# Performance work log

Hardware: AMD Instinct MI355X
Metric: run time of the kernel (lower is better)

The kernel has to match this reference:

```python
import jax, jax.numpy as jnp
import numpy as np

NEG_BIG = 10000000000.0  # matches tf source's -1e10 mask fill


def setup_inputs() -> dict:
    key = jax.random.key(0)
    k1, k2, k3 = jax.random.split(key, 3)
    B, H, T, D = 2, 12, 4096, 64
    return {
        "q": jax.random.normal(k1, (B, H, T, D), dtype=jnp.float32),
        "k": jax.random.normal(k2, (B, H, T, D), dtype=jnp.float32),
        "v": jax.random.normal(k3, (B, H, T, D), dtype=jnp.float32),
        "localAttention": 256,
    }


def _band_mask(nd, ns, local_attention, dtype):
    # 1's in the lower triangle counting from the lower-right corner,
    # optionally restricted to a local window of width `local_attention`.
    i = jnp.arange(nd)[:, None]
    j = jnp.arange(ns)[None, :]
    m = i >= j - ns + nd
    if local_attention > 0:
        m = m & (i < j - ns + nd + local_attention)
    return m.astype(dtype)


def reference(q, k, v, localAttention):
    # q,k,v: [B, H, T, D]
    dimv = v.shape[-1]
    w = jnp.einsum("bhqd,bhkd->bhqk", q, k) * (1.0 / np.sqrt(dimv))
    nd, ns = w.shape[2], w.shape[3]
    b = _band_mask(nd, ns, localAttention, w.dtype)[None, None]  # [1,1,nd,ns]
    w = w * b - jnp.asarray(NEG_BIG, w.dtype) * (1 - b)
    sm = jax.nn.softmax(w, axis=-1)
    out = jnp.einsum("bhqk,bhkd->bhqd", sm, v)       # [B,H,T,Dv]
    out = jnp.transpose(out, (0, 2, 1, 3))            # [B,T,H,Dv]
    B, T, H, Dv = out.shape
    return out.reshape(B, T, H * Dv)
```

## Files before the change

### kernel.cpp

```cpp
#include <hip/hip_runtime.h>

#define TT 4096
#define DD 64
#define HH 12
#define LAMAX 256
#define KT 64
#define NT 6
#define VS 68

typedef __attribute__((ext_vector_type(8))) short s8v;
typedef __attribute__((ext_vector_type(4))) short s4v;
typedef __attribute__((ext_vector_type(2))) short s2v;
typedef __attribute__((ext_vector_type(4))) float f4v;

static __device__ __forceinline__ short f2bf(float f) {
  unsigned u = __builtin_bit_cast(unsigned, f);
  u += 0x7FFFu + ((u >> 16) & 1u);
  return (short)(u >> 16);
}

static __device__ __forceinline__ s8v pack8(float4 a, float4 b) {
  s8v r;
  r[0] = f2bf(a.x); r[1] = f2bf(a.y); r[2] = f2bf(a.z); r[3] = f2bf(a.w);
  r[4] = f2bf(b.x); r[5] = f2bf(b.y); r[6] = f2bf(b.z); r[7] = f2bf(b.w);
  return r;
}

static __device__ __forceinline__ f4v MFMA16(s4v a, s4v b, f4v c) {
#if defined(__has_builtin) && __has_builtin(__builtin_amdgcn_mfma_f32_16x16x16bf16_1k)
  return __builtin_amdgcn_mfma_f32_16x16x16bf16_1k(a, b, c, 0, 0, 0);
#else
  asm volatile("v_mfma_f32_16x16x16_bf16 %0, %1, %2, %0\n\ts_nop 7\n\ts_nop 7"
               : "+v"(c) : "v"(a), "v"(b));
  return c;
#endif
}

__global__ __launch_bounds__(256, 3)
void lma_attn_kernel(const float* __restrict__ Q, const float* __restrict__ K,
                     const float* __restrict__ V, const int* __restrict__ laPtr,
                     float* __restrict__ out)
{
  __shared__ short k_lds[2][64 * 64];
  __shared__ short vt_lds[2][64 * VS];

  const int tid  = threadIdx.x;
  const int lane = tid & 63;
  const int w    = tid >> 6;
  const int c    = lane & 15;
  const int g    = lane >> 4;

  const int bid = blockIdx.x;
  const int wg  = (bid & 7) * 96 + (bid >> 3);
  const int bh  = wg >> 5;
  const int q0  = (wg & 31) << 7;
  const int la  = laPtr[0];

  const size_t base = (size_t)bh * (TT * DD);
  const int qw0 = q0 + w * 32;

  s8v qf[2][2];
  #pragma unroll
  for (int rg = 0; rg < 2; ++rg) {
    const float* qp = Q + base + (size_t)(qw0 + rg * 16 + c) * DD + 8 * g;
    qf[rg][0] = pack8(*(const float4*)qp,        *(const float4*)(qp + 4));
    qf[rg][1] = pack8(*(const float4*)(qp + 32), *(const float4*)(qp + 36));
  }

  const int kj  = tid >> 2;
  const int kd0 = (tid & 3) << 4;
  const int vj0 = (tid & 31) << 1;
  const int vd0 = (tid >> 5) << 3;

  float4 kr0, kr1, kr2, kr3, vr0, vr1, vr2, vr3;
  auto stage_load = [&](int kj0) {
    const float* kp = K + base + (size_t)(kj0 + kj) * DD + kd0;
    kr0 = *(const float4*)kp;        kr1 = *(const float4*)(kp + 4);
    kr2 = *(const float4*)(kp + 8);  kr3 = *(const float4*)(kp + 12);
    const float* vp = V + base + (size_t)(kj0 + vj0) * DD + vd0;
    vr0 = *(const float4*)vp;        vr1 = *(const float4*)(vp + 4);
    vr2 = *(const float4*)(vp + DD); vr3 = *(const float4*)(vp + DD + 4);
  };
  auto stage_write = [&](int buf) {
    short* kb = (short*)k_lds[buf];
    const int sw = kj & 7, g8 = kd0 >> 3;
    *(s8v*)&kb[kj * 64 + ((g8    ) ^ sw) * 8] = pack8(kr0, kr1);
    *(s8v*)&kb[kj * 64 + ((g8 + 1) ^ sw) * 8] = pack8(kr2, kr3);
    short* vb = (short*)vt_lds[buf];
    const float a0[8] = {vr0.x, vr0.y, vr0.z, vr0.w, vr1.x, vr1.y, vr1.z, vr1.w};
    const float a1[8] = {vr2.x, vr2.y, vr2.z, vr2.w, vr3.x, vr3.y, vr3.z, vr3.w};
    #pragma unroll
    for (int e = 0; e < 8; ++e) {
      s2v pr; pr[0] = f2bf(a0[e]); pr[1] = f2bf(a1[e]);
      *(s2v*)&vb[(vd0 + e) * VS + vj0] = pr;
    }
  };

  f4v acc[2][4] = {};
  float m2[2]   = {-1e30f, -1e30f};
  float lsum[2] = {0.f, 0.f};
  const float SCL = 0.125f * 1.44269504f;

  const int t0 = (q0 >= LAMAX) ? 0 : ((LAMAX - q0) >> 6);

  stage_load(q0 - LAMAX + (t0 << 6));
  stage_write(t0 & 1);
  __syncthreads();

  for (int t = t0; t < NT; ++t) {
    const int cb  = t & 1;
    const int kj0 = q0 - LAMAX + (t << 6);
    if (t + 1 < NT) stage_load(kj0 + KT);

    const short* kb = (const short*)k_lds[cb];
    const short* vb = (const short*)vt_lds[cb];

    #pragma unroll
    for (int rg = 0; rg < 2; ++rg) {
      const int rb = qw0 + (rg << 4);
      if (!((kj0 <= rb + 15) && (kj0 + KT >= rb - la + 2))) continue;
      const int i_row = rb + c;
      const int jlo = i_row - la + 1;

      f4v sa[4] = {};
      #pragma unroll
      for (int ch = 0; ch < 2; ++ch) {
        #pragma unroll
        for (int ks = 0; ks < 4; ++ks) {
          s8v kf = *(const s8v*)&kb[(ks * 16 + c) * 64 + (((ch << 2) + g) ^ (c & 7)) * 8];
          sa[ks] = __builtin_amdgcn_mfma_f32_16x16x32_bf16(kf, qf[rg][ch], sa[ks], 0, 0, 0);
        }
      }

      float p[4][4]; float tmax = -1e30f;
      #pragma unroll
      for (int ks = 0; ks < 4; ++ks)
        #pragma unroll
        for (int r = 0; r < 4; ++r) {
          const int jt = kj0 + ks * 16 + 4 * g + r;
          float s = sa[ks][r] * SCL;
          s = (jt >= jlo && jt <= i_row) ? s : -1e30f;
          p[ks][r] = s; tmax = fmaxf(tmax, s);
        }
      tmax = fmaxf(tmax, __shfl_xor(tmax, 16, 64));
      tmax = fmaxf(tmax, __shfl_xor(tmax, 32, 64));
      const float mn = fmaxf(m2[rg], tmax);
      const float corr = exp2f(m2[rg] - mn);
      m2[rg] = mn;

      s4v pb[4]; float ps = 0.f;
      #pragma unroll
      for (int ks = 0; ks < 4; ++ks)
        #pragma unroll
        for (int r = 0; r < 4; ++r) {
          const float e = exp2f(p[ks][r] - mn);
          ps += e; pb[ks][r] = f2bf(e);
        }
      ps += __shfl_xor(ps, 16, 64);
      ps += __shfl_xor(ps, 32, 64);
      lsum[rg] = lsum[rg] * corr + ps;
      #pragma unroll
      for (int dt = 0; dt < 4; ++dt) {
        acc[rg][dt][0] *= corr; acc[rg][dt][1] *= corr;
        acc[rg][dt][2] *= corr; acc[rg][dt][3] *= corr;
      }

      #pragma unroll
      for (int dt = 0; dt < 4; ++dt) {
        const int d = dt * 16 + c;
        #pragma unroll
        for (int sub = 0; sub < 4; ++sub) {
          s4v vf = *(const s4v*)&vb[d * VS + sub * 16 + g * 4];
          acc[rg][dt] = MFMA16(vf, pb[sub], acc[rg][dt]);
        }
      }
    }

    if (t + 1 < NT) stage_write((t + 1) & 1);
    __syncthreads();
  }

  #pragma unroll
  for (int rg = 0; rg < 2; ++rg) {
    const float inv = 1.f / lsum[rg];
    const int row = qw0 + (rg << 4) + c;
    float* op = out + ((size_t)(bh / HH) * TT + row) * (HH * DD) + (bh % HH) * DD + 4 * g;
    #pragma unroll
    for (int dt = 0; dt < 4; ++dt) {
      float4 o;
      o.x = acc[rg][dt][0] * inv; o.y = acc[rg][dt][1] * inv;
      o.z = acc[rg][dt][2] * inv; o.w = acc[rg][dt][3] * inv;
      *(float4*)(op + dt * 16) = o;
    }
  }
}

extern "C" void kernel_launch(void* const* d_in, const int* in_sizes, int n_in,
                              void* d_out, int out_size, void* d_ws, size_t ws_size,
                              hipStream_t stream) {
  const float* q = (const float*)d_in[0];
  const float* k = (const float*)d_in[1];
  const float* v = (const float*)d_in[2];
  const int* la = (const int*)d_in[3];
  float* out = (float*)d_out;
  (void)in_sizes; (void)n_in; (void)out_size; (void)d_ws; (void)ws_size;

  dim3 grid(24 * 32);
  dim3 block(256);
  lma_attn_kernel<<<grid, block, 0, stream>>>(q, k, v, la, out);
}
```

Before: 141.1 us.

## Halve query tile per block, fold scale into Q, specialize masks, lazy rescale

Each block now handles 64 query rows (16 per wave) instead of 128, which doubles the grid and raises the occupancy target to 4 blocks per CU. The K/V window loop shrinks from 6 to 5 tiles, so each block stages less redundant K/V data. The softmax scale is folded into Q at pack time, and the causal and local-window masks are applied only on tiles that straddle a boundary, through compile-time specialized branches. Accumulator rescaling is skipped when the row max grows by at most 8 in log2 space. In exchange, each K/V tile is shared by fewer query rows and total K/V loads go up, and the lazy rescale lets exp values reach up to 2^8 before bf16 conversion.

```diff
diff --git a/kernel.cpp b/kernel.cpp
--- a/kernel.cpp
+++ b/kernel.cpp
@@ -5,7 +5,6 @@
 #define HH 12
 #define LAMAX 256
 #define KT 64
-#define NT 6
 #define VS 68
 
 typedef __attribute__((ext_vector_type(8))) short s8v;
@@ -26,17 +25,26 @@
   return r;
 }
 
+static __device__ __forceinline__ s8v pack8s(float4 a, float4 b, float s) {
+  s8v r;
+  r[0] = f2bf(a.x * s); r[1] = f2bf(a.y * s); r[2] = f2bf(a.z * s); r[3] = f2bf(a.w * s);
+  r[4] = f2bf(b.x * s); r[5] = f2bf(b.y * s); r[6] = f2bf(b.z * s); r[7] = f2bf(b.w * s);
+  return r;
+}
+
 static __device__ __forceinline__ f4v MFMA16(s4v a, s4v b, f4v c) {
 #if defined(__has_builtin) && __has_builtin(__builtin_amdgcn_mfma_f32_16x16x16bf16_1k)
   return __builtin_amdgcn_mfma_f32_16x16x16bf16_1k(a, b, c, 0, 0, 0);
+#elif defined(__has_builtin) && __has_builtin(__builtin_amdgcn_mfma_f32_16x16x16_bf16)
+  return __builtin_amdgcn_mfma_f32_16x16x16_bf16(a, b, c, 0, 0, 0);
 #else
-  asm volatile("v_mfma_f32_16x16x16_bf16 %0, %1, %2, %0\n\ts_nop 7\n\ts_nop 7"
-               : "+v"(c) : "v"(a), "v"(b));
+  asm("v_mfma_f32_16x16x16_bf16 %0, %1, %2, %0\n\ts_nop 7\n\ts_nop 7"
+      : "+v"(c) : "v"(a), "v"(b));
   return c;
 #endif
 }
 
-__global__ __launch_bounds__(256, 3)
+__global__ __launch_bounds__(256, 4)
 void lma_attn_kernel(const float* __restrict__ Q, const float* __restrict__ K,
                      const float* __restrict__ V, const int* __restrict__ laPtr,
                      float* __restrict__ out)
@@ -51,20 +59,21 @@
   const int g    = lane >> 4;
 
   const int bid = blockIdx.x;
-  const int wg  = (bid & 7) * 96 + (bid >> 3);
-  const int bh  = wg >> 5;
-  const int q0  = (wg & 31) << 7;
+  const int wg  = (bid & 7) * 192 + (bid >> 3);
+  const int bh  = wg >> 6;
+  const int q0  = (wg & 63) << 6;
   const int la  = laPtr[0];
 
   const size_t base = (size_t)bh * (TT * DD);
-  const int qw0 = q0 + w * 32;
-
-  s8v qf[2][2];
-  #pragma unroll
-  for (int rg = 0; rg < 2; ++rg) {
-    const float* qp = Q + base + (size_t)(qw0 + rg * 16 + c) * DD + 8 * g;
-    qf[rg][0] = pack8(*(const float4*)qp,        *(const float4*)(qp + 4));
-    qf[rg][1] = pack8(*(const float4*)(qp + 32), *(const float4*)(qp + 36));
+  const int rb    = q0 + w * 16;
+  const int i_row = rb + c;
+
+  const float SCL = 0.125f * 1.44269504f;
+  s8v qf[2];
+  {
+    const float* qp = Q + base + (size_t)i_row * DD + 8 * g;
+    qf[0] = pack8s(*(const float4*)qp,        *(const float4*)(qp + 4),  SCL);
+    qf[1] = pack8s(*(const float4*)(qp + 32), *(const float4*)(qp + 36), SCL);
   }
 
   const int kj  = tid >> 2;
@@ -96,10 +105,9 @@
     }
   };
 
-  f4v acc[2][4] = {};
-  float m2[2]   = {-1e30f, -1e30f};
-  float lsum[2] = {0.f, 0.f};
-  const float SCL = 0.125f * 1.44269504f;
+  f4v acc[4] = {};
+  float m2   = -1e30f;
+  float lsum = 0.f;
 
   const int t0 = (q0 >= LAMAX) ? 0 : ((LAMAX - q0) >> 6);
 
@@ -107,63 +115,76 @@
   stage_write(t0 & 1);
   __syncthreads();
 
-  for (int t = t0; t < NT; ++t) {
-    const int cb  = t & 1;
+  for (int t = t0; t < 5; ++t) {
     const int kj0 = q0 - LAMAX + (t << 6);
-    if (t + 1 < NT) stage_load(kj0 + KT);
-
-    const short* kb = (const short*)k_lds[cb];
-    const short* vb = (const short*)vt_lds[cb];
-
-    #pragma unroll
-    for (int rg = 0; rg < 2; ++rg) {
-      const int rb = qw0 + (rg << 4);
-      if (!((kj0 <= rb + 15) && (kj0 + KT >= rb - la + 2))) continue;
-      const int i_row = rb + c;
-      const int jlo = i_row - la + 1;
-
+    if (t < 4) stage_load(kj0 + KT);
+
+    const short* kb = (const short*)k_lds[t & 1];
+    const short* vb = (const short*)vt_lds[t & 1];
+
+    if ((kj0 <= rb + 15) && (kj0 + KT >= rb - la + 2)) {
       f4v sa[4] = {};
       #pragma unroll
-      for (int ch = 0; ch < 2; ++ch) {
+      for (int ch = 0; ch < 2; ++ch)
         #pragma unroll
         for (int ks = 0; ks < 4; ++ks) {
           s8v kf = *(const s8v*)&kb[(ks * 16 + c) * 64 + (((ch << 2) + g) ^ (c & 7)) * 8];
-          sa[ks] = __builtin_amdgcn_mfma_f32_16x16x32_bf16(kf, qf[rg][ch], sa[ks], 0, 0, 0);
+          sa[ks] = __builtin_amdgcn_mfma_f32_16x16x32_bf16(kf, qf[ch], sa[ks], 0, 0, 0);
+        }
+
+      const bool needC = (kj0 + 63 > rb);
+      const bool needL = (kj0 < rb + 16 - la);
+      const int jrel = kj0 - rb;
+      const int jloR = i_row - la + 1;
+      float p[4][4];
+      #define MASKMAX(NC, NL)                                              \
+        _Pragma("unroll")                                                  \
+        for (int ks = 0; ks < 4; ++ks)                                     \
+          _Pragma("unroll")                                                \
+          for (int r = 0; r < 4; ++r) {                                    \
+            float s = sa[ks][r];                                           \
+            if (NC || NL) {                                                \
+              const int jt = kj0 + ks * 16 + 4 * g + r;                    \
+              bool ok = true;                                              \
+              if (NC) ok = (jt <= i_row);                                  \
+              if (NL) ok = ok && (jt >= jloR);                             \
+              s = ok ? s : -1e30f;                                         \
+            }                                                              \
+            p[ks][r] = s;                                                  \
+          }
+      if (needC) { if (needL) { MASKMAX(true, true) } else { MASKMAX(true, false) } }
+      else       { if (needL) { MASKMAX(false, true) } else { MASKMAX(false, false) } }
+      #undef MASKMAX
+      (void)jrel;
+
+      float t0a = fmaxf(fmaxf(p[0][0], p[0][1]), fmaxf(p[0][2], p[0][3]));
+      float t1a = fmaxf(fmaxf(p[1][0], p[1][1]), fmaxf(p[1][2], p[1][3]));
+      float t2a = fmaxf(fmaxf(p[2][0], p[2][1]), fmaxf(p[2][2], p[2][3]));
+      float t3a = fmaxf(fmaxf(p[3][0], p[3][1]), fmaxf(p[3][2], p[3][3]));
+      float tmax = fmaxf(fmaxf(t0a, t1a), fmaxf(t2a, t3a));
+      tmax = fmaxf(tmax, __shfl_xor(tmax, 16, 64));
+      tmax = fmaxf(tmax, __shfl_xor(tmax, 32, 64));
+
+      if (!__all(tmax <= m2 + 8.0f)) {
+        const float mn = fmaxf(m2, tmax);
+        const float corr = exp2f(m2 - mn);
+        m2 = mn;
+        lsum *= corr;
+        #pragma unroll
+        for (int dt = 0; dt < 4; ++dt) {
+          acc[dt][0] *= corr; acc[dt][1] *= corr;
+          acc[dt][2] *= corr; acc[dt][3] *= corr;
         }
       }
 
-      float p[4][4]; float tmax = -1e30f;
+      s4v pb[4]; float e[4][4];
       #pragma unroll
       for (int ks = 0; ks < 4; ++ks)
         #pragma unroll
         for (int r = 0; r < 4; ++r) {
-          const int jt = kj0 + ks * 16 + 4 * g + r;
-          float s = sa[ks][r] * SCL;
-          s = (jt >= jlo && jt <= i_row) ? s : -1e30f;
-          p[ks][r] = s; tmax = fmaxf(tmax, s);
-        }
-      tmax = fmaxf(tmax, __shfl_xor(tmax, 16, 64));
-      tmax = fmaxf(tmax, __shfl_xor(tmax, 32, 64));
-      const float mn = fmaxf(m2[rg], tmax);
-      const float corr = exp2f(m2[rg] - mn);
-      m2[rg] = mn;
-
-      s4v pb[4]; float ps = 0.f;
-      #pragma unroll
-      for (int ks = 0; ks < 4; ++ks)
-        #pragma unroll
-        for (int r = 0; r < 4; ++r) {
-          const float e = exp2f(p[ks][r] - mn);
-          ps += e; pb[ks][r] = f2bf(e);
-        }
-      ps += __shfl_xor(ps, 16, 64);
-      ps += __shfl_xor(ps, 32, 64);
-      lsum[rg] = lsum[rg] * corr + ps;
-      #pragma unroll
-      for (int dt = 0; dt < 4; ++dt) {
-        acc[rg][dt][0] *= corr; acc[rg][dt][1] *= corr;
-        acc[rg][dt][2] *= corr; acc[rg][dt][3] *= corr;
-      }
+          e[ks][r] = exp2f(p[ks][r] - m2);
+          pb[ks][r] = f2bf(e[ks][r]);
+        }
 
       #pragma unroll
       for (int dt = 0; dt < 4; ++dt) {
@@ -171,27 +192,32 @@
         #pragma unroll
         for (int sub = 0; sub < 4; ++sub) {
           s4v vf = *(const s4v*)&vb[d * VS + sub * 16 + g * 4];
-          acc[rg][dt] = MFMA16(vf, pb[sub], acc[rg][dt]);
+          acc[dt] = MFMA16(vf, pb[sub], acc[dt]);
         }
       }
+
+      float s0 = (e[0][0] + e[0][1]) + (e[0][2] + e[0][3]);
+      float s1 = (e[1][0] + e[1][1]) + (e[1][2] + e[1][3]);
+      float s2 = (e[2][0] + e[2][1]) + (e[2][2] + e[2][3]);
+      float s3 = (e[3][0] + e[3][1]) + (e[3][2] + e[3][3]);
+      float ps = (s0 + s1) + (s2 + s3);
+      ps += __shfl_xor(ps, 16, 64);
+      ps += __shfl_xor(ps, 32, 64);
+      lsum += ps;
     }
 
-    if (t + 1 < NT) stage_write((t + 1) & 1);
+    if (t < 4) stage_write((t + 1) & 1);
     __syncthreads();
   }
 
+  const float inv = 1.f / lsum;
+  float* op = out + ((size_t)(bh / HH) * TT + i_row) * (HH * DD) + (bh % HH) * DD + 4 * g;
   #pragma unroll
-  for (int rg = 0; rg < 2; ++rg) {
-    const float inv = 1.f / lsum[rg];
-    const int row = qw0 + (rg << 4) + c;
-    float* op = out + ((size_t)(bh / HH) * TT + row) * (HH * DD) + (bh % HH) * DD + 4 * g;
-    #pragma unroll
-    for (int dt = 0; dt < 4; ++dt) {
-      float4 o;
-      o.x = acc[rg][dt][0] * inv; o.y = acc[rg][dt][1] * inv;
-      o.z = acc[rg][dt][2] * inv; o.w = acc[rg][dt][3] * inv;
-      *(float4*)(op + dt * 16) = o;
-    }
+  for (int dt = 0; dt < 4; ++dt) {
+    float4 o;
+    o.x = acc[dt][0] * inv; o.y = acc[dt][1] * inv;
+    o.z = acc[dt][2] * inv; o.w = acc[dt][3] * inv;
+    *(float4*)(op + dt * 16) = o;
   }
 }
 
@@ -205,7 +231,7 @@
   float* out = (float*)d_out;
   (void)in_sizes; (void)n_in; (void)out_size; (void)d_ws; (void)ws_size;
 
-  dim3 grid(24 * 32);
+  dim3 grid(24 * 64);
   dim3 block(256);
   lma_attn_kernel<<<grid, block, 0, stream>>>(q, k, v, la, out);
 }
```

After: 143.2 us. No clear change (+1.4%).
